# Optimization experiments

Hardware: AMD Instinct MI355X
Metric: run time of the kernel (lower is better)

The kernel has to match this reference:

```python
import math
import jax, jax.numpy as jnp
import numpy as np

# dims (match init_kwargs)
N, K = 10000, 32            # nodes, padded neighbors per node
IN_F, H, HEADS = 128, 128, 8
T_F, R_F, OUT, LAYERS = 64, 32, 64, 2
HD = H // HEADS
START_T, END_T = 0.25, 0.75
ATTN_NORM = math.sqrt(1.0 / HD)
T_NORM = math.sqrt(1.0 / (T_F // 2))
EPS = 1e-5


def layernorm(x, g, b):
    m = jnp.mean(x, axis=-1, keepdims=True)
    v = jnp.var(x, axis=-1, keepdims=True)
    return (x - m) * jax.lax.rsqrt(v + EPS) * g + b


def t2v(dt, Wt, bt):
    # TimeKernel: linear(1->T_F/2) then interleaved [sin, cos] * norm
    h = dt[..., None] * Wt + bt                      # [..., T_F/2]
    return jnp.stack([jnp.sin(h), jnp.cos(h)], axis=-1).reshape(*h.shape[:-1], T_F) * T_NORM


def tgat_layer(x, neighbors, times, rels, mask,
               Wkqv, Wt, bt, Wtime, Wedge, g1, b1n, g2, b2n, W1, bl1, W2, bl2):
    xn = layernorm(x, g1, b1n)
    kqv = xn @ Wkqv                                  # [N, 3H], chunk order (k, q, v)
    k_, q_, v_ = jnp.split(kqv, 3, axis=1)
    kn = k_[neighbors]                               # [N, K, H] irregular gather
    vn = v_[neighbors]
    # per-node time reference: max over [start_t; masked times] (times>=start_t so start_t covered)
    tmax = jnp.max(jnp.where(mask, times, START_T), axis=1)        # [N]
    tq_emb = t2v(tmax - START_T, Wt, bt)             # [N, T_F] (the prepended start_t row)
    tn_emb = t2v(tmax[:, None] - times, Wt, bt)      # [N, K, T_F]
    t_qq = (tq_emb @ Wtime)[:, H:2 * H]              # query chunk of time KQV
    tkn = tn_emb @ Wtime                             # [N, K, 3H]
    re = rels @ Wedge                                # [N, K, 3H]
    q = q_ + t_qq                                    # [N, H]
    k = kn + tkn[..., :H] + re[..., :H]
    v = vn + tkn[..., 2 * H:] + re[..., 2 * H:]
    qh = q.reshape(N, HEADS, HD)
    kh = k.reshape(N, K, HEADS, HD)
    vh = v.reshape(N, K, HEADS, HD)
    scores = jnp.einsum('nhd,nkhd->nhk', qh, kh) * ATTN_NORM
    scores = jnp.where(mask[:, None, :], scores, -1e30)
    attn = jax.nn.softmax(scores, axis=-1)
    out = jnp.einsum('nhk,nkhd->nhd', attn, vh).reshape(N, H)
    has = jnp.any(mask, axis=1)                      # nodes with zero valid neighbors -> zeros
    h = jnp.where(has[:, None], out, 0.0)
    h2 = h + xn
    hn = layernorm(h2, g2, b2n)
    z = jnp.concatenate([xn, hn], axis=1)
    z = jax.nn.relu(z @ W1 + bl1) @ W2 + bl2
    return z + h2


def setup_inputs() -> dict:
    key = jax.random.key(0)
    ks = jax.random.split(key, 16)
    w = lambda i, *shape: jax.random.normal(ks[i], shape, dtype=jnp.float32) * 0.05
    return {
        'x': jax.random.normal(ks[0], (N, IN_F), dtype=jnp.float32),
        'neighbors': jax.random.randint(ks[1], (N, K), 0, N, dtype=jnp.int32),
        'times': jax.random.uniform(ks[2], (N, K), dtype=jnp.float32),
        'rels': jax.random.normal(ks[3], (N, K, R_F), dtype=jnp.float32),
        'Wp': w(4, IN_F, H), 'bp': jnp.zeros((H,), jnp.float32),
        'Wkqv': w(5, H, 3 * H),
        'Wt': w(6, T_F // 2), 'bt': jnp.zeros((T_F // 2,), jnp.float32),
        'Wtime': w(7, T_F, 3 * H),
        'Wedge': w(8, R_F, 3 * H),
        'g1': jnp.ones((H,), jnp.float32), 'b1n': jnp.zeros((H,), jnp.float32),
        'g2': jnp.ones((H,), jnp.float32), 'b2n': jnp.zeros((H,), jnp.float32),
        'W1': w(9, 2 * H, H), 'bl1': jnp.zeros((H,), jnp.float32),
        'W2': w(10, H, H), 'bl2': jnp.zeros((H,), jnp.float32),
        'Wo': w(11, H, OUT), 'bo': jnp.zeros((OUT,), jnp.float32),
    }


def reference(x, neighbors, times, rels, Wp, bp, Wkqv, Wt, bt, Wtime, Wedge,
              g1, b1n, g2, b2n, W1, bl1, W2, bl2, Wo, bo):
    mask = (times >= START_T) & (times < END_T)      # [N, K] temporal neighbor mask
    h = jax.nn.relu(x @ Wp + bp)
    for _ in range(LAYERS):                          # layers SHARE weights (ModuleList([layer]*layers))
        h = tgat_layer(h, neighbors, times, rels, mask,
                       Wkqv, Wt, bt, Wtime, Wedge, g1, b1n, g2, b2n, W1, bl1, W2, bl2)
    return h @ Wo + bo
```

## Files before the change

kernel.cpp:

```cpp
#include <hip/hip_runtime.h>
#include <hip/hip_bf16.h>

#define NN 10000
#define KK 32
#define HH 128
#define TFH 32
#define RFE 32
#define OUTF 64
#define START_T 0.25f
#define END_T 0.75f
#define ATTN_NORM 0.25f
#define T_NORM 0.17677669529663687f
#define LN_EPS 1e-5f
#define MT 64

typedef __attribute__((ext_vector_type(4))) float f32x4;
typedef __attribute__((ext_vector_type(8))) short bf16x8;

__device__ __forceinline__ ushort f2bf(float x){
  __hip_bfloat16 b = __float2bfloat16(x);
  return *(ushort*)&b;
}
__device__ __forceinline__ float bf2f(ushort u){
  __hip_bfloat16 b = *(__hip_bfloat16*)&u;
  return __bfloat162float(b);
}

__device__ __forceinline__ float groupsum32(float v){
  v += __shfl_xor(v, 16, 32);
  v += __shfl_xor(v, 8, 32);
  v += __shfl_xor(v, 4, 32);
  v += __shfl_xor(v, 2, 32);
  v += __shfl_xor(v, 1, 32);
  return v;
}

__device__ __forceinline__ float halfsum(float v, float* red, int nn, int wv){
  #pragma unroll
  for (int off=32; off; off>>=1) v += __shfl_down(v, off, 64);
  __syncthreads();
  if ((threadIdx.x & 63)==0) red[wv] = v;
  __syncthreads();
  return red[nn*2] + red[nn*2+1];
}

__global__ __launch_bounds__(256) void k_prep_wT(const float* __restrict__ Wp, const float* __restrict__ Wkqv,
    const float* __restrict__ W1, const float* __restrict__ W2, const float* __restrict__ Wo,
    ushort* __restrict__ WpT, ushort* __restrict__ WkqvT, ushort* __restrict__ W1T,
    ushort* __restrict__ W2T, ushort* __restrict__ WoT){
  int id = blockIdx.x*256 + threadIdx.x;
  if (id < 16384){ int n=id>>7, k=id&127; WpT[id]=f2bf(Wp[k*HH+n]); return; }
  id -= 16384;
  if (id < 49152){ int n=id>>7, k=id&127; WkqvT[id]=f2bf(Wkqv[k*384+n]); return; }
  id -= 49152;
  if (id < 32768){ int n=id>>8, k=id&255; W1T[id]=f2bf(W1[k*HH+n]); return; }
  id -= 32768;
  if (id < 16384){ int n=id>>7, k=id&127; W2T[id]=f2bf(W2[k*HH+n]); return; }
  id -= 16384;
  if (id < 8192){ int n=id>>7, k=id&127; WoT[id]=f2bf(Wo[k*OUTF+n]); }
}

__global__ __launch_bounds__(256) void k_prep_w(const float* __restrict__ Wtime, const float* __restrict__ Wedge,
                                                ushort* __restrict__ WcT){
  const int r = blockIdx.x, c = threadIdx.x;
  const int cc = (c < 128) ? c : (c + 128);
  const float v = (r < 64) ? Wtime[r*384 + cc] : Wedge[(r-64)*384 + cc];
  WcT[c*96 + r] = f2bf(v);
}

#define LDA1 136
__global__ __launch_bounds__(256) void k_proj_mfma(const float* __restrict__ X, const ushort* __restrict__ WpT,
                                                   const float* __restrict__ bp, float* __restrict__ Y){
  __shared__ ushort As[16*LDA1];
  const int tid = threadIdx.x, n0 = blockIdx.x*16;
  #pragma unroll
  for (int p=0;p<2;++p){
    const int idx = tid + p*256;
    const int row = idx>>5, c4 = (idx&31)*4;
    const float4 v = *(const float4*)&X[(size_t)(n0+row)*HH + c4];
    *(ushort4*)&As[row*LDA1 + c4] = make_ushort4(f2bf(v.x), f2bf(v.y), f2bf(v.z), f2bf(v.w));
  }
  __syncthreads();
  const int w = tid>>6, lane = tid&63;
  const int lr = lane&15, lk8 = (lane>>4)*8, rbase = (lane>>4)*4;
  bf16x8 a[4];
  #pragma unroll
  for (int kk=0;kk<4;kk++) a[kk] = *(const bf16x8*)&As[lr*LDA1 + kk*32 + lk8];
  f32x4 acc[2];
  #pragma unroll
  for (int nt=0;nt<2;nt++) acc[nt] = (f32x4){0.f,0.f,0.f,0.f};
  #pragma unroll
  for (int nt=0;nt<2;nt++){
    const int n = w*2 + nt;
    #pragma unroll
    for (int kk=0;kk<4;kk++){
      bf16x8 b = *(const bf16x8*)&WpT[(n*16+lr)*HH + kk*32 + lk8];
      acc[nt] = __builtin_amdgcn_mfma_f32_16x16x32_bf16(a[kk], b, acc[nt],0,0,0);
    }
  }
  #pragma unroll
  for (int nt=0;nt<2;nt++){
    const int c = (w*2+nt)*16 + lr;
    const float bj = bp[c];
    #pragma unroll
    for (int r=0;r<4;r++)
      Y[(size_t)(n0 + rbase + r)*HH + c] = fmaxf(acc[nt][r] + bj, 0.f);
  }
}

__global__ __launch_bounds__(128) void k_prep_node(const float* __restrict__ times, const float* __restrict__ Wt,
                                                   const float* __restrict__ bt, const float* __restrict__ Wtime,
                                                   const int* __restrict__ nbrs,
                                                   float* __restrict__ tqq, float* __restrict__ tmaxb,
                                                   int* __restrict__ cntb, uint* __restrict__ vmaskb,
                                                   int* __restrict__ nbrC){
  __shared__ float temb[2*TFH];
  __shared__ float tm_sh;
  const int n = blockIdx.x, j = threadIdx.x;
  if (j < KK){
    float t = times[n*KK + j];
    bool valid = (t >= START_T) && (t < END_T);
    float val = valid ? t : START_T;
    #pragma unroll
    for (int off=16; off; off>>=1) val = fmaxf(val, __shfl_xor(val, off, 32));
    if (j==0){ tm_sh = val; tmaxb[n] = val; }
    const uint vm = (uint)__ballot(valid);
    if (valid){
      const int slot = __popc(vm & ((1u<<j)-1));
      nbrC[n*KK + slot] = nbrs[n*KK + j];
    }
    if (j==0){ cntb[n] = __popc(vm); vmaskb[n] = vm; }
  }
  __syncthreads();
  if (j < TFH){
    float hh = fmaf(tm_sh - START_T, Wt[j], bt[j]);
    temb[2*j]   = __sinf(hh)*T_NORM;
    temb[2*j+1] = __cosf(hh)*T_NORM;
  }
  __syncthreads();
  float acc = 0.f;
  #pragma unroll
  for (int f=0; f<2*TFH; f++) acc = fmaf(temb[f], Wtime[f*384 + HH + j], acc);
  tqq[n*HH + j] = acc;
}

#define LDA 104
#define LDKV 264
__global__ __launch_bounds__(256) void k_prep_kv4(
    const float* __restrict__ times, const float* __restrict__ rels, const float* __restrict__ tmaxb,
    const float* __restrict__ Wt, const float* __restrict__ bt, const ushort* __restrict__ WcT,
    const uint* __restrict__ vmaskb, uint4* __restrict__ kvout){
  __shared__ ushort smem[MT*LDKV];
  __shared__ float dt_sh[MT];
  ushort* Fa = smem;
  ushort* kvs = smem;
  const int tid = threadIdx.x;
  const int node0 = blockIdx.x*2;
  if (tid < MT){
    const int node = node0 + (tid>>5);
    dt_sh[tid] = tmaxb[node] - times[node*KK + (tid&31)];
  }
  __syncthreads();
  #pragma unroll
  for (int s0=0; s0<8; ++s0){
    const int s = tid + s0*256;
    const int p = s>>5, f = s&31;
    const float hh = fmaf(dt_sh[p], Wt[f], bt[f]);
    ushort2 pk;
    pk.x = f2bf(__sinf(hh)*T_NORM);
    pk.y = f2bf(__cosf(hh)*T_NORM);
    *(ushort2*)&Fa[p*LDA + 2*f] = pk;
  }
  #pragma unroll
  for (int s0=0; s0<2; ++s0){
    const int i = tid + s0*256;
    const int p = i>>3, seg = i&7;
    const float4 rv = *(const float4*)&rels[((size_t)node0*KK + p)*RFE + seg*4];
    ushort4 w2; w2.x=f2bf(rv.x); w2.y=f2bf(rv.y); w2.z=f2bf(rv.z); w2.w=f2bf(rv.w);
    *(ushort4*)&Fa[p*LDA + 64 + seg*4] = w2;
  }
  __syncthreads();
  const int wave = tid>>6, lane = tid&63;
  const int lr = lane&15, lk = (lane>>4)*8;
  f32x4 acc[4][4];
  #pragma unroll
  for (int m=0;m<4;m++)
    #pragma unroll
    for (int n=0;n<4;n++) acc[m][n] = (f32x4){0.f,0.f,0.f,0.f};
  #pragma unroll
  for (int kk=0; kk<3; ++kk){
    const int k0 = kk*32;
    bf16x8 a[4], b[4];
    #pragma unroll
    for (int m=0;m<4;m++) a[m] = *(const bf16x8*)&Fa[(m*16 + lr)*LDA + k0 + lk];
    #pragma unroll
    for (int n=0;n<4;n++) b[n] = *(const bf16x8*)&WcT[(wave*64 + n*16 + lr)*96 + k0 + lk];
    #pragma unroll
    for (int m=0;m<4;m++)
      #pragma unroll
      for (int n=0;n<4;n++)
        acc[m][n] = __builtin_amdgcn_mfma_f32_16x16x32_bf16(a[m], b[n], acc[m][n], 0,0,0);
  }
  __syncthreads();
  const int rbase = (lane>>4)*4;
  #pragma unroll
  for (int n=0;n<4;n++){
    const int c = wave*64 + n*16 + lr;
    const int ip = (c < 128) ? (2*c) : (2*(c-128)+1);
    #pragma unroll
    for (int m=0;m<4;m++)
      #pragma unroll
      for (int r=0;r<4;r++)
        kvs[(m*16 + rbase + r)*LDKV + ip] = f2bf(acc[m][n][r]);
  }
  __syncthreads();
  const uint vm0 = vmaskb[node0], vm1 = vmaskb[node0+1];
  #pragma unroll
  for (int pass=0; pass<8; ++pass){
    const int idx = pass*256 + tid;
    const int row = idx>>5, seg = idx&31;
    const int nloc = row>>5, k = row&31;
    const uint vm = nloc ? vm1 : vm0;
    if ((vm>>k)&1u){
      const int slot = __popc(vm & ((1u<<k)-1));
      const uint4 v = *(const uint4*)&kvs[row*LDKV + seg*8];
      kvout[((size_t)(node0+nloc)*KK + slot)*32 + seg] = v;
    }
  }
}

__global__ __launch_bounds__(256) void k_ln_kqv_mfma(const float* __restrict__ Hin, const ushort* __restrict__ WkqvT,
    const float* __restrict__ g1, const float* __restrict__ b1, const float* __restrict__ tqq,
    float* __restrict__ XN, ushort* __restrict__ xnb,
    float* __restrict__ Qf, ushort* __restrict__ KVb){
  __shared__ ushort As[16*LDA1];
  const int tid = threadIdx.x, n0 = blockIdx.x*16;
  const int grp = tid>>5, gl = tid&31;
  {
    const float4 gv = *(const float4*)&g1[gl*4];
    const float4 bv = *(const float4*)&b1[gl*4];
    #pragma unroll
    for (int rr=0; rr<2; ++rr){
      const int row = grp + rr*8;
      const int node = n0 + row;
      float4 hv = *(const float4*)&Hin[(size_t)node*HH + gl*4];
      float s = hv.x+hv.y+hv.z+hv.w;
      s = groupsum32(s);
      const float mean = s*(1.f/HH);
      const float dx=hv.x-mean, dy=hv.y-mean, dz=hv.z-mean, dw=hv.w-mean;
      float vs = dx*dx+dy*dy+dz*dz+dw*dw;
      vs = groupsum32(vs);
      const float rstd = rsqrtf(vs*(1.f/HH)+LN_EPS);
      const float x0=dx*rstd*gv.x+bv.x, x1=dy*rstd*gv.y+bv.y, x2=dz*rstd*gv.z+bv.z, x3=dw*rstd*gv.w+bv.w;
      ushort4 pk = make_ushort4(f2bf(x0), f2bf(x1), f2bf(x2), f2bf(x3));
      *(ushort4*)&As[row*LDA1 + gl*4] = pk;
      *(float4*)&XN[(size_t)node*HH + gl*4] = make_float4(x0,x1,x2,x3);
      *(ushort4*)&xnb[(size_t)node*HH + gl*4] = pk;
    }
  }
  __syncthreads();
  const int w = tid>>6, lane = tid&63;
  const int lr = lane&15, lk8 = (lane>>4)*8, rbase = (lane>>4)*4;
  bf16x8 a[4];
  #pragma unroll
  for (int kk=0;kk<4;kk++) a[kk] = *(const bf16x8*)&As[lr*LDA1 + kk*32 + lk8];
  f32x4 acc[6];
  #pragma unroll
  for (int nt=0;nt<6;nt++) acc[nt] = (f32x4){0.f,0.f,0.f,0.f};
  #pragma unroll
  for (int nt=0;nt<6;nt++){
    const int n = w*6 + nt;
    #pragma unroll
    for (int kk=0;kk<4;kk++){
      bf16x8 b = *(const bf16x8*)&WkqvT[(n*16+lr)*HH + kk*32 + lk8];
      acc[nt] = __builtin_amdgcn_mfma_f32_16x16x32_bf16(a[kk], b, acc[nt],0,0,0);
    }
  }
  #pragma unroll
  for (int nt=0;nt<6;nt++){
    const int c = (w*6+nt)*16 + lr;
    #pragma unroll
    for (int r=0;r<4;r++){
      const int node = n0 + rbase + r;
      const float v = acc[nt][r];
      if (c < HH)           KVb[(size_t)node*256 + 2*c] = f2bf(v);
      else if (c < 2*HH)    Qf[(size_t)node*HH + (c-HH)] = v + tqq[(size_t)node*HH + (c-HH)];
      else                  KVb[(size_t)node*256 + 2*(c-2*HH) + 1] = f2bf(v);
    }
  }
}

__global__ __launch_bounds__(256) void k_attn5(
    const float* __restrict__ Qf, const uint* __restrict__ KVu, const uint* __restrict__ kvaddC,
    const int* __restrict__ nbrC, const int* __restrict__ cntb,
    const float* __restrict__ XN, const float* __restrict__ g2, const float* __restrict__ b2,
    float* __restrict__ H2, ushort* __restrict__ hnb){
  __shared__ int nbr_sh[MT];
  __shared__ float red[4];
  const int tid = threadIdx.x, node0 = blockIdx.x*2;
  if (tid < MT) nbr_sh[tid] = nbrC[(node0 + (tid>>5))*KK + (tid&31)];
  __syncthreads();
  const int nn = tid>>7, j = tid&127, wv = tid>>6;
  const int node = node0 + nn;
  const int cnt = cntb[node];
  const float qs = Qf[(size_t)node*HH + j] * ATTN_NORM;
  const uint* karow = kvaddC + (size_t)node*KK*128 + j;
  float m_ = -3.0e38f, l = 0.f, accv = 0.f;
  const int cc = (cnt + 7) >> 3;
  for (int ch=0; ch<cc; ++ch){
    const int base = ch*8;
    uint ka[8], kb[8];
    #pragma unroll
    for (int i=0;i<8;i++){
      int slot = base + i; slot = (slot < cnt) ? slot : (cnt-1);
      ka[i] = karow[(size_t)slot*128];
      kb[i] = KVu[(size_t)nbr_sh[nn*32+slot]*128 + j];
    }
    float s[8];
    #pragma unroll
    for (int i=0;i<8;i++){
      float p = qs * (bf2f((ushort)(kb[i]&0xffff)) + bf2f((ushort)(ka[i]&0xffff)));
      p += __shfl_xor(p, 8, 16);
      p += __shfl_xor(p, 4, 16);
      p += __shfl_xor(p, 2, 16);
      p += __shfl_xor(p, 1, 16);
      s[i] = (base + i < cnt) ? p : -1e30f;
    }
    float cm = s[0];
    #pragma unroll
    for (int i=1;i<8;i++) cm = fmaxf(cm, s[i]);
    const float mn = fmaxf(m_, cm);
    const float sc = __expf(m_ - mn);
    l *= sc; accv *= sc;
    #pragma unroll
    for (int i=0;i<8;i++){
      const float e = __expf(s[i] - mn);
      l += e;
      accv = fmaf(e, bf2f((ushort)(kb[i]>>16)) + bf2f((ushort)(ka[i]>>16)), accv);
    }
    m_ = mn;
  }
  const float o = (cnt > 0) ? (accv / l) : 0.f;
  const float h2v = o + XN[(size_t)node*HH + j];
  H2[(size_t)node*HH + j] = h2v;
  const float mn2 = halfsum(h2v, red, nn, wv)*(1.f/HH);
  const float d = h2v - mn2;
  const float var = halfsum(d*d, red, nn, wv)*(1.f/HH);
  const float hnv = d*rsqrtf(var + LN_EPS)*g2[j] + b2[j];
  hnb[(size_t)node*HH + j] = f2bf(hnv);
}

#define LDA2 264
__global__ __launch_bounds__(256) void k_ffn_mfma(const ushort* __restrict__ xnb, const ushort* __restrict__ hnb,
    const float* __restrict__ H2, const ushort* __restrict__ W1T, const float* __restrict__ bl1,
    const ushort* __restrict__ W2T, const float* __restrict__ bl2, float* __restrict__ HOUT){
  __shared__ ushort As[16*LDA2];
  __shared__ ushort Ms[16*LDA1];
  const int tid = threadIdx.x, n0 = blockIdx.x*16;
  {
    const int row = tid>>4, c8 = (tid&15)*8;
    *(uint4*)&As[row*LDA2 + c8]       = *(const uint4*)&xnb[(size_t)(n0+row)*HH + c8];
    *(uint4*)&As[row*LDA2 + 128 + c8] = *(const uint4*)&hnb[(size_t)(n0+row)*HH + c8];
  }
  __syncthreads();
  const int w = tid>>6, lane = tid&63;
  const int lr = lane&15, lk8 = (lane>>4)*8, rbase = (lane>>4)*4;
  {
    bf16x8 a[8];
    #pragma unroll
    for (int kk=0;kk<8;kk++) a[kk] = *(const bf16x8*)&As[lr*LDA2 + kk*32 + lk8];
    f32x4 acc[2];
    #pragma unroll
    for (int nt=0;nt<2;nt++) acc[nt] = (f32x4){0.f,0.f,0.f,0.f};
    #pragma unroll
    for (int nt=0;nt<2;nt++){
      const int n = w*2 + nt;
      #pragma unroll
      for (int kk=0;kk<8;kk++){
        bf16x8 b = *(const bf16x8*)&W1T[(n*16+lr)*256 + kk*32 + lk8];
        acc[nt] = __builtin_amdgcn_mfma_f32_16x16x32_bf16(a[kk], b, acc[nt],0,0,0);
      }
    }
    #pragma unroll
    for (int nt=0;nt<2;nt++){
      const int c = (w*2+nt)*16 + lr;
      const float bj = bl1[c];
      #pragma unroll
      for (int r=0;r<4;r++)
        Ms[(rbase+r)*LDA1 + c] = f2bf(fmaxf(acc[nt][r] + bj, 0.f));
    }
  }
  __syncthreads();
  {
    bf16x8 a[4];
    #pragma unroll
    for (int kk=0;kk<4;kk++) a[kk] = *(const bf16x8*)&Ms[lr*LDA1 + kk*32 + lk8];
    f32x4 acc[2];
    #pragma unroll
    for (int nt=0;nt<2;nt++) acc[nt] = (f32x4){0.f,0.f,0.f,0.f};
    #pragma unroll
    for (int nt=0;nt<2;nt++){
      const int n = w*2 + nt;
      #pragma unroll
      for (int kk=0;kk<4;kk++){
        bf16x8 b = *(const bf16x8*)&W2T[(n*16+lr)*HH + kk*32 + lk8];
        acc[nt] = __builtin_amdgcn_mfma_f32_16x16x32_bf16(a[kk], b, acc[nt],0,0,0);
      }
    }
    #pragma unroll
    for (int nt=0;nt<2;nt++){
      const int c = (w*2+nt)*16 + lr;
      const float bj = bl2[c];
      #pragma unroll
      for (int r=0;r<4;r++){
        const size_t node = n0 + rbase + r;
        HOUT[node*HH + c] = acc[nt][r] + bj + H2[node*HH + c];
      }
    }
  }
}

__global__ __launch_bounds__(256) void k_out_mfma(const float* __restrict__ Hin, const ushort* __restrict__ WoT,
                                                  const float* __restrict__ bo, float* __restrict__ OUT){
  __shared__ ushort As[16*LDA1];
  const int tid = threadIdx.x, n0 = blockIdx.x*16;
  #pragma unroll
  for (int p=0;p<2;++p){
    const int idx = tid + p*256;
    const int row = idx>>5, c4 = (idx&31)*4;
    const float4 v = *(const float4*)&Hin[(size_t)(n0+row)*HH + c4];
    *(ushort4*)&As[row*LDA1 + c4] = make_ushort4(f2bf(v.x), f2bf(v.y), f2bf(v.z), f2bf(v.w));
  }
  __syncthreads();
  const int w = tid>>6, lane = tid&63;
  const int lr = lane&15, lk8 = (lane>>4)*8, rbase = (lane>>4)*4;
  bf16x8 a[4];
  #pragma unroll
  for (int kk=0;kk<4;kk++) a[kk] = *(const bf16x8*)&As[lr*LDA1 + kk*32 + lk8];
  f32x4 acc = (f32x4){0.f,0.f,0.f,0.f};
  #pragma unroll
  for (int kk=0;kk<4;kk++){
    bf16x8 b = *(const bf16x8*)&WoT[(w*16+lr)*HH + kk*32 + lk8];
    acc = __builtin_amdgcn_mfma_f32_16x16x32_bf16(a[kk], b, acc,0,0,0);
  }
  const int c = w*16 + lr;
  const float bj = bo[c];
  #pragma unroll
  for (int r=0;r<4;r++)
    OUT[(size_t)(n0 + rbase + r)*OUTF + c] = acc[r] + bj;
}

extern "C" void kernel_launch(void* const* d_in, const int* in_sizes, int n_in,
                              void* d_out, int out_size, void* d_ws, size_t ws_size,
                              hipStream_t stream){
  const float* x         = (const float*)d_in[0];
  const int*   neighbors = (const int*)  d_in[1];
  const float* times     = (const float*)d_in[2];
  const float* rels      = (const float*)d_in[3];
  const float* Wp        = (const float*)d_in[4];
  const float* bp        = (const float*)d_in[5];
  const float* Wkqv      = (const float*)d_in[6];
  const float* Wt        = (const float*)d_in[7];
  const float* bt        = (const float*)d_in[8];
  const float* Wtime     = (const float*)d_in[9];
  const float* Wedge     = (const float*)d_in[10];
  const float* g1        = (const float*)d_in[11];
  const float* b1n       = (const float*)d_in[12];
  const float* g2        = (const float*)d_in[13];
  const float* b2n       = (const float*)d_in[14];
  const float* W1        = (const float*)d_in[15];
  const float* bl1       = (const float*)d_in[16];
  const float* W2        = (const float*)d_in[17];
  const float* bl2       = (const float*)d_in[18];
  const float* Wo        = (const float*)d_in[19];
  const float* bo        = (const float*)d_in[20];
  float* out = (float*)d_out;

  char* ws = (char*)d_ws;
  size_t off = 0;
  auto carve = [&](size_t bytes)->char*{
    char* p = ws + off; off = (off + bytes + 255) & ~(size_t)255; return p;
  };
  float* hA    = (float*)carve((size_t)NN*HH*4);
  float* hB    = (float*)carve((size_t)NN*HH*4);
  float* xn    = (float*)carve((size_t)NN*HH*4);
  float* h2    = (float*)carve((size_t)NN*HH*4);
  float* tqq   = (float*)carve((size_t)NN*HH*4);
  float* Qfp   = (float*)carve((size_t)NN*HH*4);
  float* tmaxb = (float*)carve((size_t)NN*4);
  int*   cntb  = (int*)carve((size_t)NN*4);
  uint*  vmaskb= (uint*)carve((size_t)NN*4);
  int*   nbrC  = (int*)carve((size_t)NN*KK*4);
  ushort* KVb  = (ushort*)carve((size_t)NN*256*2);
  ushort* xnb  = (ushort*)carve((size_t)NN*HH*2);
  ushort* hnb  = (ushort*)carve((size_t)NN*HH*2);
  ushort* WcTg = (ushort*)carve((size_t)256*96*2);
  ushort* WpT  = (ushort*)carve((size_t)16384*2);
  ushort* WkqvT= (ushort*)carve((size_t)49152*2);
  ushort* W1T  = (ushort*)carve((size_t)32768*2);
  ushort* W2T  = (ushort*)carve((size_t)16384*2);
  ushort* WoT  = (ushort*)carve((size_t)8192*2);
  uint*   kvaddC = (uint*)carve((size_t)NN*KK*256*2);
  (void)ws_size;

  k_prep_wT<<<480, 256, 0, stream>>>(Wp, Wkqv, W1, W2, Wo, WpT, WkqvT, W1T, W2T, WoT);
  k_prep_w<<<96, 256, 0, stream>>>(Wtime, Wedge, WcTg);
  k_proj_mfma<<<NN/16, 256, 0, stream>>>(x, WpT, bp, hA);
  k_prep_node<<<NN, 128, 0, stream>>>(times, Wt, bt, Wtime, neighbors,
                                      tqq, tmaxb, cntb, vmaskb, nbrC);
  k_prep_kv4<<<NN/2, 256, 0, stream>>>(times, rels, tmaxb, Wt, bt, WcTg, vmaskb, (uint4*)kvaddC);

  float* cur = hA; float* nxt = hB;
  for (int layer=0; layer<2; ++layer){
    k_ln_kqv_mfma<<<NN/16, 256, 0, stream>>>(cur, WkqvT, g1, b1n, tqq, xn, xnb, Qfp, KVb);
    k_attn5<<<NN/2, 256, 0, stream>>>(Qfp, (const uint*)KVb, kvaddC, nbrC, cntb,
                                      xn, g2, b2n, h2, hnb);
    k_ffn_mfma<<<NN/16, 256, 0, stream>>>(xnb, hnb, h2, W1T, bl1, W2T, bl2, nxt);
    float* t = cur; cur = nxt; nxt = t;
  }
  k_out_mfma<<<NN/16, 256, 0, stream>>>(cur, WoT, bo, out);
}
```

Before: 185.7 us.

## Compact valid neighbor pairs before time/edge KV projection and merge weight prep

The node-prep kernel now writes compacted per-slot time deltas and original pair indices, so the KV-add prep kernel only builds features and runs MFMA tiles for valid neighbor rows, skipping 16-row tiles beyond the valid count. The B-operand weight fragments are hoisted into registers once. The separate Wtime/Wedge transpose kernel is folded into the main weight prep kernel to save a launch. It adds two scratch arrays and leaves behind an unused dead kernel (k_prep_kv5), and the per-row gather of rels is now indirect.

Result: slower. 190.3 us (+2.4%).

```diff
diff --git a/kernel.cpp b/kernel.cpp
--- a/kernel.cpp
+++ b/kernel.cpp
@@ -46,8 +46,9 @@
 
 __global__ __launch_bounds__(256) void k_prep_wT(const float* __restrict__ Wp, const float* __restrict__ Wkqv,
     const float* __restrict__ W1, const float* __restrict__ W2, const float* __restrict__ Wo,
+    const float* __restrict__ Wtime, const float* __restrict__ Wedge,
     ushort* __restrict__ WpT, ushort* __restrict__ WkqvT, ushort* __restrict__ W1T,
-    ushort* __restrict__ W2T, ushort* __restrict__ WoT){
+    ushort* __restrict__ W2T, ushort* __restrict__ WoT, ushort* __restrict__ WcT){
   int id = blockIdx.x*256 + threadIdx.x;
   if (id < 16384){ int n=id>>7, k=id&127; WpT[id]=f2bf(Wp[k*HH+n]); return; }
   id -= 16384;
@@ -57,15 +58,14 @@
   id -= 32768;
   if (id < 16384){ int n=id>>7, k=id&127; W2T[id]=f2bf(W2[k*HH+n]); return; }
   id -= 16384;
-  if (id < 8192){ int n=id>>7, k=id&127; WoT[id]=f2bf(Wo[k*OUTF+n]); }
-}
-
-__global__ __launch_bounds__(256) void k_prep_w(const float* __restrict__ Wtime, const float* __restrict__ Wedge,
-                                                ushort* __restrict__ WcT){
-  const int r = blockIdx.x, c = threadIdx.x;
-  const int cc = (c < 128) ? c : (c + 128);
-  const float v = (r < 64) ? Wtime[r*384 + cc] : Wedge[(r-64)*384 + cc];
-  WcT[c*96 + r] = f2bf(v);
+  if (id < 8192){ int n=id>>7, k=id&127; WoT[id]=f2bf(Wo[k*OUTF+n]); return; }
+  id -= 8192;
+  if (id < 24576){
+    const int c = id/96, r = id%96;
+    const int cc = (c < 128) ? c : (c + 128);
+    const float v = (r < 64) ? Wtime[r*384 + cc] : Wedge[(r-64)*384 + cc];
+    WcT[c*96 + r] = f2bf(v);
+  }
 }
 
 #define LDA1 136
@@ -112,8 +112,8 @@
                                                    const float* __restrict__ bt, const float* __restrict__ Wtime,
                                                    const int* __restrict__ nbrs,
                                                    float* __restrict__ tqq, float* __restrict__ tmaxb,
-                                                   int* __restrict__ cntb, uint* __restrict__ vmaskb,
-                                                   int* __restrict__ nbrC){
+                                                   int* __restrict__ cntb, int* __restrict__ nbrC,
+                                                   float* __restrict__ dtC, int* __restrict__ pairC){
   __shared__ float temb[2*TFH];
   __shared__ float tm_sh;
   const int n = blockIdx.x, j = threadIdx.x;
@@ -128,8 +128,10 @@
     if (valid){
       const int slot = __popc(vm & ((1u<<j)-1));
       nbrC[n*KK + slot] = nbrs[n*KK + j];
-    }
-    if (j==0){ cntb[n] = __popc(vm); vmaskb[n] = vm; }
+      dtC[n*KK + slot]  = val - t;
+      pairC[n*KK + slot]= j;
+    }
+    if (j==0) cntb[n] = __popc(vm);
   }
   __syncthreads();
   if (j < TFH){
@@ -146,85 +148,136 @@
 
 #define LDA 104
 #define LDKV 264
-__global__ __launch_bounds__(256) void k_prep_kv4(
-    const float* __restrict__ times, const float* __restrict__ rels, const float* __restrict__ tmaxb,
-    const float* __restrict__ Wt, const float* __restrict__ bt, const ushort* __restrict__ WcT,
-    const uint* __restrict__ vmaskb, uint4* __restrict__ kvout){
+__global__ __launch_bounds__(256) void k_prep_kv5(
+    const float* __restrict__ dtC, const int* __restrict__ pairC, const int* __restrict__ cntb,
+    const float* __restrict__ rels, const ushort* __restrict__ WcT,
+    uint4* __restrict__ kvout){
   __shared__ ushort smem[MT*LDKV];
   __shared__ float dt_sh[MT];
+  __shared__ int pair_sh[MT];
   ushort* Fa = smem;
   ushort* kvs = smem;
   const int tid = threadIdx.x;
   const int node0 = blockIdx.x*2;
-  if (tid < MT){
-    const int node = node0 + (tid>>5);
-    dt_sh[tid] = tmaxb[node] - times[node*KK + (tid&31)];
+  const int cnt0 = cntb[node0], cnt1 = cntb[node0+1];
+  const int R = cnt0 + cnt1;
+  if (R == 0) return;
+  if (tid < MT && tid < R){
+    const int i = (tid >= cnt0) ? 1 : 0;
+    const int s = tid - (i ? cnt0 : 0);
+    const int node = node0 + i;
+    dt_sh[tid]   = dtC[node*KK + s];
+    pair_sh[tid] = node*KK + pairC[node*KK + s];
   }
   __syncthreads();
   #pragma unroll
   for (int s0=0; s0<8; ++s0){
     const int s = tid + s0*256;
     const int p = s>>5, f = s&31;
-    const float hh = fmaf(dt_sh[p], Wt[f], bt[f]);
-    ushort2 pk;
-    pk.x = f2bf(__sinf(hh)*T_NORM);
-    pk.y = f2bf(__cosf(hh)*T_NORM);
-    *(ushort2*)&Fa[p*LDA + 2*f] = pk;
+    if (p < R){
+      const float hh = dt_sh[p] * __ldg(&((const float*)nullptr == nullptr ? dtC : dtC)[0]) * 0.f + dt_sh[p];
+    }
+  }
+  __syncthreads();
+  (void)Fa; (void)kvs; (void)pair_sh;
+}
+
+__global__ __launch_bounds__(256) void k_prep_kv5r(
+    const float* __restrict__ dtC, const int* __restrict__ pairC, const int* __restrict__ cntb,
+    const float* __restrict__ rels, const float* __restrict__ Wt, const float* __restrict__ bt,
+    const ushort* __restrict__ WcT, uint4* __restrict__ kvout){
+  __shared__ ushort smem[MT*LDKV];
+  __shared__ float dt_sh[MT];
+  __shared__ int pair_sh[MT];
+  ushort* Fa = smem;
+  ushort* kvs = smem;
+  const int tid = threadIdx.x;
+  const int node0 = blockIdx.x*2;
+  const int cnt0 = cntb[node0], cnt1 = cntb[node0+1];
+  const int R = cnt0 + cnt1;
+  if (R == 0) return;
+  if (tid < MT && tid < R){
+    const int i = (tid >= cnt0) ? 1 : 0;
+    const int s = tid - (i ? cnt0 : 0);
+    const int node = node0 + i;
+    dt_sh[tid]   = dtC[node*KK + s];
+    pair_sh[tid] = node*KK + pairC[node*KK + s];
+  }
+  __syncthreads();
+  #pragma unroll
+  for (int s0=0; s0<8; ++s0){
+    const int s = tid + s0*256;
+    const int p = s>>5, f = s&31;
+    if (p < R){
+      const float hh = fmaf(dt_sh[p], Wt[f], bt[f]);
+      ushort2 pk;
+      pk.x = f2bf(__sinf(hh)*T_NORM);
+      pk.y = f2bf(__cosf(hh)*T_NORM);
+      *(ushort2*)&Fa[p*LDA + 2*f] = pk;
+    }
   }
   #pragma unroll
   for (int s0=0; s0<2; ++s0){
     const int i = tid + s0*256;
     const int p = i>>3, seg = i&7;
-    const float4 rv = *(const float4*)&rels[((size_t)node0*KK + p)*RFE + seg*4];
-    ushort4 w2; w2.x=f2bf(rv.x); w2.y=f2bf(rv.y); w2.z=f2bf(rv.z); w2.w=f2bf(rv.w);
-    *(ushort4*)&Fa[p*LDA + 64 + seg*4] = w2;
+    if (p < R){
+      const float4 rv = *(const float4*)&rels[(size_t)pair_sh[p]*RFE + seg*4];
+      ushort4 w2; w2.x=f2bf(rv.x); w2.y=f2bf(rv.y); w2.z=f2bf(rv.z); w2.w=f2bf(rv.w);
+      *(ushort4*)&Fa[p*LDA + 64 + seg*4] = w2;
+    }
   }
   __syncthreads();
   const int wave = tid>>6, lane = tid&63;
   const int lr = lane&15, lk = (lane>>4)*8;
+  bf16x8 bfr[3][4];
+  #pragma unroll
+  for (int kk=0;kk<3;kk++)
+    #pragma unroll
+    for (int n=0;n<4;n++)
+      bfr[kk][n] = *(const bf16x8*)&WcT[(wave*64 + n*16 + lr)*96 + kk*32 + lk];
   f32x4 acc[4][4];
   #pragma unroll
   for (int m=0;m<4;m++)
     #pragma unroll
     for (int n=0;n<4;n++) acc[m][n] = (f32x4){0.f,0.f,0.f,0.f};
   #pragma unroll
-  for (int kk=0; kk<3; ++kk){
-    const int k0 = kk*32;
-    bf16x8 a[4], b[4];
-    #pragma unroll
-    for (int m=0;m<4;m++) a[m] = *(const bf16x8*)&Fa[(m*16 + lr)*LDA + k0 + lk];
-    #pragma unroll
-    for (int n=0;n<4;n++) b[n] = *(const bf16x8*)&WcT[(wave*64 + n*16 + lr)*96 + k0 + lk];
-    #pragma unroll
-    for (int m=0;m<4;m++)
-      #pragma unroll
-      for (int n=0;n<4;n++)
-        acc[m][n] = __builtin_amdgcn_mfma_f32_16x16x32_bf16(a[m], b[n], acc[m][n], 0,0,0);
+  for (int m=0;m<4;m++){
+    if (m*16 < R){
+      bf16x8 a[3];
+      #pragma unroll
+      for (int kk=0;kk<3;kk++) a[kk] = *(const bf16x8*)&Fa[(m*16 + lr)*LDA + kk*32 + lk];
+      #pragma unroll
+      for (int kk=0;kk<3;kk++)
+        #pragma unroll
+        for (int n=0;n<4;n++)
+          acc[m][n] = __builtin_amdgcn_mfma_f32_16x16x32_bf16(a[kk], bfr[kk][n], acc[m][n], 0,0,0);
+    }
   }
   __syncthreads();
   const int rbase = (lane>>4)*4;
   #pragma unroll
-  for (int n=0;n<4;n++){
-    const int c = wave*64 + n*16 + lr;
-    const int ip = (c < 128) ? (2*c) : (2*(c-128)+1);
-    #pragma unroll
-    for (int m=0;m<4;m++)
-      #pragma unroll
-      for (int r=0;r<4;r++)
-        kvs[(m*16 + rbase + r)*LDKV + ip] = f2bf(acc[m][n][r]);
-  }
-  __syncthreads();
-  const uint vm0 = vmaskb[node0], vm1 = vmaskb[node0+1];
+  for (int m=0;m<4;m++){
+    if (m*16 < R){
+      #pragma unroll
+      for (int n=0;n<4;n++){
+        const int c = wave*64 + n*16 + lr;
+        const int ip = (c < 128) ? (2*c) : (2*(c-128)+1);
+        #pragma unroll
+        for (int r=0;r<4;r++)
+          kvs[(m*16 + rbase + r)*LDKV + ip] = f2bf(acc[m][n][r]);
+      }
+    }
+  }
+  __syncthreads();
   #pragma unroll
   for (int pass=0; pass<8; ++pass){
     const int idx = pass*256 + tid;
     const int row = idx>>5, seg = idx&31;
-    const int nloc = row>>5, k = row&31;
-    const uint vm = nloc ? vm1 : vm0;
-    if ((vm>>k)&1u){
-      const int slot = __popc(vm & ((1u<<k)-1));
+    if (row < R){
+      const int i = (row >= cnt0) ? 1 : 0;
+      const int s = row - (i ? cnt0 : 0);
       const uint4 v = *(const uint4*)&kvs[row*LDKV + seg*8];
-      kvout[((size_t)(node0+nloc)*KK + slot)*32 + seg] = v;
+      kvout[((size_t)(node0+i)*KK + s)*32 + seg] = v;
     }
   }
 }
@@ -489,8 +542,9 @@
   float* Qfp   = (float*)carve((size_t)NN*HH*4);
   float* tmaxb = (float*)carve((size_t)NN*4);
   int*   cntb  = (int*)carve((size_t)NN*4);
-  uint*  vmaskb= (uint*)carve((size_t)NN*4);
   int*   nbrC  = (int*)carve((size_t)NN*KK*4);
+  float* dtC   = (float*)carve((size_t)NN*KK*4);
+  int*   pairC = (int*)carve((size_t)NN*KK*4);
   ushort* KVb  = (ushort*)carve((size_t)NN*256*2);
   ushort* xnb  = (ushort*)carve((size_t)NN*HH*2);
   ushort* hnb  = (ushort*)carve((size_t)NN*HH*2);
@@ -503,12 +557,12 @@
   uint*   kvaddC = (uint*)carve((size_t)NN*KK*256*2);
   (void)ws_size;
 
-  k_prep_wT<<<480, 256, 0, stream>>>(Wp, Wkqv, W1, W2, Wo, WpT, WkqvT, W1T, W2T, WoT);
-  k_prep_w<<<96, 256, 0, stream>>>(Wtime, Wedge, WcTg);
+  k_prep_wT<<<576, 256, 0, stream>>>(Wp, Wkqv, W1, W2, Wo, Wtime, Wedge,
+                                     WpT, WkqvT, W1T, W2T, WoT, WcTg);
   k_proj_mfma<<<NN/16, 256, 0, stream>>>(x, WpT, bp, hA);
   k_prep_node<<<NN, 128, 0, stream>>>(times, Wt, bt, Wtime, neighbors,
-                                      tqq, tmaxb, cntb, vmaskb, nbrC);
-  k_prep_kv4<<<NN/2, 256, 0, stream>>>(times, rels, tmaxb, Wt, bt, WcTg, vmaskb, (uint4*)kvaddC);
+                                      tqq, tmaxb, cntb, nbrC, dtC, pairC);
+  k_prep_kv5r<<<NN/2, 256, 0, stream>>>(dtC, pairC, cntb, rels, Wt, bt, WcTg, (uint4*)kvaddC);
 
   float* cur = hA; float* nxt = hB;
   for (int layer=0; layer<2; ++layer){
```

## Map one wavefront per node in attention with 2 channels per lane

Applied to the files above, without the earlier changes.

The attention kernel now processes four nodes per block, one 64-lane wavefront per node, with each lane handling two adjacent channels through 8-byte loads. This shortens the shuffle reduction for head dot products and replaces the shared-memory, syncthreads-based layernorm reduction with a pure wave-level xor shuffle. The two weight-prep kernels are also merged into one launch. The trade-off is more registers per lane and fewer blocks in the grid.

Result: faster. 179.1 us (-3.6%).

```diff
diff --git a/kernel.cpp b/kernel.cpp
--- a/kernel.cpp
+++ b/kernel.cpp
@@ -35,19 +35,21 @@
   return v;
 }
 
-__device__ __forceinline__ float halfsum(float v, float* red, int nn, int wv){
-  #pragma unroll
-  for (int off=32; off; off>>=1) v += __shfl_down(v, off, 64);
-  __syncthreads();
-  if ((threadIdx.x & 63)==0) red[wv] = v;
-  __syncthreads();
-  return red[nn*2] + red[nn*2+1];
+__device__ __forceinline__ float wavesum64(float v){
+  v += __shfl_xor(v, 32, 64);
+  v += __shfl_xor(v, 16, 64);
+  v += __shfl_xor(v, 8, 64);
+  v += __shfl_xor(v, 4, 64);
+  v += __shfl_xor(v, 2, 64);
+  v += __shfl_xor(v, 1, 64);
+  return v;
 }
 
 __global__ __launch_bounds__(256) void k_prep_wT(const float* __restrict__ Wp, const float* __restrict__ Wkqv,
     const float* __restrict__ W1, const float* __restrict__ W2, const float* __restrict__ Wo,
+    const float* __restrict__ Wtime, const float* __restrict__ Wedge,
     ushort* __restrict__ WpT, ushort* __restrict__ WkqvT, ushort* __restrict__ W1T,
-    ushort* __restrict__ W2T, ushort* __restrict__ WoT){
+    ushort* __restrict__ W2T, ushort* __restrict__ WoT, ushort* __restrict__ WcT){
   int id = blockIdx.x*256 + threadIdx.x;
   if (id < 16384){ int n=id>>7, k=id&127; WpT[id]=f2bf(Wp[k*HH+n]); return; }
   id -= 16384;
@@ -57,15 +59,14 @@
   id -= 32768;
   if (id < 16384){ int n=id>>7, k=id&127; W2T[id]=f2bf(W2[k*HH+n]); return; }
   id -= 16384;
-  if (id < 8192){ int n=id>>7, k=id&127; WoT[id]=f2bf(Wo[k*OUTF+n]); }
-}
-
-__global__ __launch_bounds__(256) void k_prep_w(const float* __restrict__ Wtime, const float* __restrict__ Wedge,
-                                                ushort* __restrict__ WcT){
-  const int r = blockIdx.x, c = threadIdx.x;
-  const int cc = (c < 128) ? c : (c + 128);
-  const float v = (r < 64) ? Wtime[r*384 + cc] : Wedge[(r-64)*384 + cc];
-  WcT[c*96 + r] = f2bf(v);
+  if (id < 8192){ int n=id>>7, k=id&127; WoT[id]=f2bf(Wo[k*OUTF+n]); return; }
+  id -= 8192;
+  if (id < 24576){
+    const int c = id/96, r = id%96;
+    const int cc = (c < 128) ? c : (c + 128);
+    const float v = (r < 64) ? Wtime[r*384 + cc] : Wedge[(r-64)*384 + cc];
+    WcT[c*96 + r] = f2bf(v);
+  }
 }
 
 #define LDA1 136
@@ -290,40 +291,40 @@
   }
 }
 
-__global__ __launch_bounds__(256) void k_attn5(
-    const float* __restrict__ Qf, const uint* __restrict__ KVu, const uint* __restrict__ kvaddC,
+__global__ __launch_bounds__(256) void k_attn6(
+    const float* __restrict__ Qf, const uint2* __restrict__ KVu2, const uint2* __restrict__ kvaddC2,
     const int* __restrict__ nbrC, const int* __restrict__ cntb,
     const float* __restrict__ XN, const float* __restrict__ g2, const float* __restrict__ b2,
     float* __restrict__ H2, ushort* __restrict__ hnb){
-  __shared__ int nbr_sh[MT];
-  __shared__ float red[4];
-  const int tid = threadIdx.x, node0 = blockIdx.x*2;
-  if (tid < MT) nbr_sh[tid] = nbrC[(node0 + (tid>>5))*KK + (tid&31)];
-  __syncthreads();
-  const int nn = tid>>7, j = tid&127, wv = tid>>6;
-  const int node = node0 + nn;
+  __shared__ int nbr_sh[4][KK];
+  const int tid = threadIdx.x, node0 = blockIdx.x*4;
+  if (tid < 128) nbr_sh[tid>>5][tid&31] = nbrC[(node0 + (tid>>5))*KK + (tid&31)];
+  __syncthreads();
+  const int wv = tid>>6, l = tid&63;
+  const int node = node0 + wv;
   const int cnt = cntb[node];
-  const float qs = Qf[(size_t)node*HH + j] * ATTN_NORM;
-  const uint* karow = kvaddC + (size_t)node*KK*128 + j;
-  float m_ = -3.0e38f, l = 0.f, accv = 0.f;
+  const float2 q2 = *(const float2*)&Qf[(size_t)node*HH + 2*l];
+  const float q0s = q2.x * ATTN_NORM, q1s = q2.y * ATTN_NORM;
+  const uint2* karow = kvaddC2 + (size_t)node*KK*64 + l;
+  float m_ = -3.0e38f, sume = 0.f, a0 = 0.f, a1 = 0.f;
   const int cc = (cnt + 7) >> 3;
   for (int ch=0; ch<cc; ++ch){
     const int base = ch*8;
-    uint ka[8], kb[8];
+    uint2 ka[8], kb[8];
     #pragma unroll
     for (int i=0;i<8;i++){
       int slot = base + i; slot = (slot < cnt) ? slot : (cnt-1);
-      ka[i] = karow[(size_t)slot*128];
-      kb[i] = KVu[(size_t)nbr_sh[nn*32+slot]*128 + j];
+      ka[i] = karow[(size_t)slot*64];
+      kb[i] = KVu2[(size_t)nbr_sh[wv][slot]*64 + l];
     }
     float s[8];
     #pragma unroll
     for (int i=0;i<8;i++){
-      float p = qs * (bf2f((ushort)(kb[i]&0xffff)) + bf2f((ushort)(ka[i]&0xffff)));
-      p += __shfl_xor(p, 8, 16);
-      p += __shfl_xor(p, 4, 16);
-      p += __shfl_xor(p, 2, 16);
-      p += __shfl_xor(p, 1, 16);
+      float p = q0s * (bf2f((ushort)(kb[i].x&0xffff)) + bf2f((ushort)(ka[i].x&0xffff)))
+              + q1s * (bf2f((ushort)(kb[i].y&0xffff)) + bf2f((ushort)(ka[i].y&0xffff)));
+      p += __shfl_xor(p, 4, 8);
+      p += __shfl_xor(p, 2, 8);
+      p += __shfl_xor(p, 1, 8);
       s[i] = (base + i < cnt) ? p : -1e30f;
     }
     float cm = s[0];
@@ -331,23 +332,31 @@
     for (int i=1;i<8;i++) cm = fmaxf(cm, s[i]);
     const float mn = fmaxf(m_, cm);
     const float sc = __expf(m_ - mn);
-    l *= sc; accv *= sc;
+    sume *= sc; a0 *= sc; a1 *= sc;
     #pragma unroll
     for (int i=0;i<8;i++){
       const float e = __expf(s[i] - mn);
-      l += e;
-      accv = fmaf(e, bf2f((ushort)(kb[i]>>16)) + bf2f((ushort)(ka[i]>>16)), accv);
+      sume += e;
+      a0 = fmaf(e, bf2f((ushort)(kb[i].x>>16)) + bf2f((ushort)(ka[i].x>>16)), a0);
+      a1 = fmaf(e, bf2f((ushort)(kb[i].y>>16)) + bf2f((ushort)(ka[i].y>>16)), a1);
     }
     m_ = mn;
   }
-  const float o = (cnt > 0) ? (accv / l) : 0.f;
-  const float h2v = o + XN[(size_t)node*HH + j];
-  H2[(size_t)node*HH + j] = h2v;
-  const float mn2 = halfsum(h2v, red, nn, wv)*(1.f/HH);
-  const float d = h2v - mn2;
-  const float var = halfsum(d*d, red, nn, wv)*(1.f/HH);
-  const float hnv = d*rsqrtf(var + LN_EPS)*g2[j] + b2[j];
-  hnb[(size_t)node*HH + j] = f2bf(hnv);
+  const float inv = (cnt > 0) ? (1.f / sume) : 0.f;
+  const float2 xn2 = *(const float2*)&XN[(size_t)node*HH + 2*l];
+  const float h0 = a0*inv + xn2.x;
+  const float h1 = a1*inv + xn2.y;
+  *(float2*)&H2[(size_t)node*HH + 2*l] = make_float2(h0, h1);
+  const float mean = wavesum64(h0 + h1) * (1.f/HH);
+  const float d0 = h0 - mean, d1 = h1 - mean;
+  const float var = wavesum64(d0*d0 + d1*d1) * (1.f/HH);
+  const float rstd = rsqrtf(var + LN_EPS);
+  const float2 gv = *(const float2*)&g2[2*l];
+  const float2 bv = *(const float2*)&b2[2*l];
+  ushort2 hn;
+  hn.x = f2bf(d0*rstd*gv.x + bv.x);
+  hn.y = f2bf(d1*rstd*gv.y + bv.y);
+  *(ushort2*)&hnb[(size_t)node*HH + 2*l] = hn;
 }
 
 #define LDA2 264
@@ -490,7 +499,7 @@
   float* tmaxb = (float*)carve((size_t)NN*4);
   int*   cntb  = (int*)carve((size_t)NN*4);
   uint*  vmaskb= (uint*)carve((size_t)NN*4);
-  int*   nbrC  = (int*)carve((size_t)NN*KK*4);
+  int*   nbrC  = (int*)carve((size_t)(NN+4)*KK*4);
   ushort* KVb  = (ushort*)carve((size_t)NN*256*2);
   ushort* xnb  = (ushort*)carve((size_t)NN*HH*2);
   ushort* hnb  = (ushort*)carve((size_t)NN*HH*2);
@@ -503,8 +512,8 @@
   uint*   kvaddC = (uint*)carve((size_t)NN*KK*256*2);
   (void)ws_size;
 
-  k_prep_wT<<<480, 256, 0, stream>>>(Wp, Wkqv, W1, W2, Wo, WpT, WkqvT, W1T, W2T, WoT);
-  k_prep_w<<<96, 256, 0, stream>>>(Wtime, Wedge, WcTg);
+  k_prep_wT<<<576, 256, 0, stream>>>(Wp, Wkqv, W1, W2, Wo, Wtime, Wedge,
+                                     WpT, WkqvT, W1T, W2T, WoT, WcTg);
   k_proj_mfma<<<NN/16, 256, 0, stream>>>(x, WpT, bp, hA);
   k_prep_node<<<NN, 128, 0, stream>>>(times, Wt, bt, Wtime, neighbors,
                                       tqq, tmaxb, cntb, vmaskb, nbrC);
@@ -513,7 +522,7 @@
   float* cur = hA; float* nxt = hB;
   for (int layer=0; layer<2; ++layer){
     k_ln_kqv_mfma<<<NN/16, 256, 0, stream>>>(cur, WkqvT, g1, b1n, tqq, xn, xnb, Qfp, KVb);
-    k_attn5<<<NN/2, 256, 0, stream>>>(Qfp, (const uint*)KVb, kvaddC, nbrC, cntb,
+    k_attn6<<<NN/4, 256, 0, stream>>>(Qfp, (const uint2*)KVb, (const uint2*)kvaddC, nbrC, cntb,
                                       xn, g2, b2n, h2, hnb);
     k_ffn_mfma<<<NN/16, 256, 0, stream>>>(xnb, hnb, h2, W1T, bl1, W2T, bl2, nxt);
     float* t = cur; cur = nxt; nxt = t;
```
